# Kernel tuning notes

Measured on AMD Instinct MI355X. Metric: run time of the kernel, lower is better.

## Reference

```python
import jax, jax.numpy as jnp
import numpy as np

N = 50000   # nodes
R = 3       # relations
E = 300000  # edges per relation
H, D = 4, 32  # heads, per-head dim (hidden_feat=128)
IN, HID, OUT = 128, 128, 64
SLOPE = 0.2  # DGL GATConv leaky_relu negative slope


def setup_inputs() -> dict:
    key = jax.random.key(0)
    ks = jax.random.split(key, 12)
    s = 0.05
    return {
        "x": jax.random.normal(ks[0], (N, IN), jnp.float32),
        "edges": jax.random.randint(ks[1], (R, 2, E), 0, N, jnp.int64),
        "W1": jax.random.normal(ks[2], (R, IN, H * D), jnp.float32) * s,
        "al1": jax.random.normal(ks[3], (R, H, D), jnp.float32) * s,
        "ar1": jax.random.normal(ks[4], (R, H, D), jnp.float32) * s,
        "b1": jnp.zeros((R, H, D), jnp.float32),
        "W2": jax.random.normal(ks[5], (R, HID, H * D), jnp.float32) * s,
        "al2": jax.random.normal(ks[6], (R, H, D), jnp.float32) * s,
        "ar2": jax.random.normal(ks[7], (R, H, D), jnp.float32) * s,
        "b2": jnp.zeros((R, H, D), jnp.float32),
        "Wl": jax.random.normal(ks[8], (HID, OUT), jnp.float32) * s,
        "bl": jnp.zeros((OUT,), jnp.float32),
    }


def rgat_layer(h, edges, W, al, ar, b):
    """HeteroGraphConv(sum) of per-relation GATConv. h: [N,F]. Returns [N,H,D]."""
    out = jnp.zeros((N, H, D), h.dtype)
    for r in range(R):  # small fixed relation count
        src, dst = edges[r, 0], edges[r, 1]
        feat = (h @ W[r]).reshape(N, H, D)                  # per-relation projection
        el = jnp.einsum("nhd,hd->nh", feat, al[r])          # [N,H]
        er = jnp.einsum("nhd,hd->nh", feat, ar[r])          # [N,H]
        e = jax.nn.leaky_relu(el[src] + er[dst], SLOPE)      # [E,H]
        # edge softmax over incoming edges per destination node
        emax = jax.ops.segment_max(e, dst, num_segments=N)   # [N,H]
        ex = jnp.exp(e - emax[dst])
        denom = jax.ops.segment_sum(ex, dst, num_segments=N) # [N,H]
        alpha = ex / denom[dst]                               # [E,H]
        msg = feat[src] * alpha[:, :, None]                   # [E,H,D]
        out = out + jax.ops.segment_sum(msg, dst, num_segments=N) + b[r]
    return out


def reference(x, edges, W1, al1, ar1, b1, W2, al2, ar2, b2, Wl, bl):
    h = rgat_layer(x, edges, W1, al1, ar1, b1).reshape(N, H * D)
    h = jax.nn.relu(h)  # dropout is identity in eval mode
    h = rgat_layer(h, edges, W2, al2, ar2, b2).reshape(N, H * D)
    return h @ Wl + bl  # [N, OUT]
```

## Files before the change

### kernel.cpp

```cpp
#include <hip/hip_runtime.h>
#include <hip/hip_bf16.h>
#include <hip/hip_fp16.h>

#define Nn 50000
#define RR 3
#define EE 300000

typedef __attribute__((ext_vector_type(8))) short short8;
typedef __attribute__((ext_vector_type(4))) short short4v;
typedef __attribute__((ext_vector_type(4))) float floatx4;

__device__ __forceinline__ short f2bf(float f) {
    __hip_bfloat16 h = __float2bfloat16(f);
    return *reinterpret_cast<short*>(&h);
}


__global__ void init_kernel(const float* __restrict__ W1, const float* __restrict__ W2,
                            short* __restrict__ Z, int* __restrict__ counts,
                            int* __restrict__ totals) {
    int bx = blockIdx.x;
    if (bx < 586) {
        int i = bx * 256 + threadIdx.x;
        if (i < RR * Nn) counts[i] = 0;
        if (i < 4) totals[i] = 0;
    } else {
        int idx = (bx - 586) * 256 + threadIdx.x;
        if (idx >= 12288) return;
        int lane = idx & 63;
        int nt = (idx >> 6) & 7;
        int kt = (idx >> 9) & 3;
        int rl = idx >> 11;
        int layer = rl / 3, r = rl % 3;
        const float* W = (layer ? W2 : W1) + (size_t)r * 16384;
        int n = nt * 16 + (lane & 15);
        int k0 = kt * 32 + (lane >> 4) * 8;
        short8 v;
        #pragma unroll
        for (int j = 0; j < 8; ++j) v[j] = f2bf(W[(size_t)(k0 + j) * 128 + n]);
        *(short8*)&Z[(size_t)idx * 8] = v;
    }
}


__global__ void count_kernel(const int* __restrict__ edges, int* __restrict__ counts,
                             int* __restrict__ ord) {
    int i = blockIdx.x * blockDim.x + threadIdx.x;
    if (i >= RR * EE / 4) return;
    int g = i * 4;
    int r = g / EE, e0 = g - r * EE;
    int4 d = *(const int4*)&edges[(size_t)r * 2 * EE + EE + e0];
    int* cb = counts + r * Nn;
    int4 o;
    o.x = atomicAdd(&cb[d.x], 1);
    o.y = atomicAdd(&cb[d.y], 1);
    o.z = atomicAdd(&cb[d.z], 1);
    o.w = atomicAdd(&cb[d.w], 1);
    *(int4*)&ord[g] = o;
}

__global__ __launch_bounds__(256) void alloc_kernel(const int* __restrict__ counts,
                                                    int* __restrict__ row_start,
                                                    int* __restrict__ totals) {
    __shared__ int s[256];
    __shared__ int base_s;
    int r = blockIdx.y;
    int tid = threadIdx.x;
    int n = blockIdx.x * 256 + tid;
    int idx = r * Nn + n;
    int c = (n < Nn) ? counts[idx] : 0;
    s[tid] = c;
    __syncthreads();
    #pragma unroll
    for (int off = 1; off < 256; off <<= 1) {
        int v = 0;
        if (tid >= off) v = s[tid - off];
        __syncthreads();
        if (tid >= off) s[tid] += v;
        __syncthreads();
    }
    if (tid == 255) base_s = atomicAdd(&totals[r], s[255]);
    __syncthreads();
    if (n < Nn) row_start[idx] = base_s + s[tid] - c;
}

__global__ void scatter_kernel(const int* __restrict__ edges, const int* __restrict__ ord,
                               const int* __restrict__ row_start,
                               int* __restrict__ csr_s, int* __restrict__ csr_d) {
    int i = blockIdx.x * blockDim.x + threadIdx.x;
    if (i >= RR * EE / 4) return;
    int g = i * 4;
    int r = g / EE, e0 = g - r * EE;
    int4 s4 = *(const int4*)&edges[(size_t)r * 2 * EE + e0];
    int4 d4 = *(const int4*)&edges[(size_t)r * 2 * EE + EE + e0];
    int4 o4 = *(const int4*)&ord[g];
    const int* rs = row_start + r * Nn;
    int* cs = csr_s + (size_t)r * EE;
    int* cd = csr_d + (size_t)r * EE;
    int p0 = rs[d4.x] + o4.x, p1 = rs[d4.y] + o4.y;
    int p2 = rs[d4.z] + o4.z, p3 = rs[d4.w] + o4.w;
    cs[p0] = s4.x; cs[p1] = s4.y; cs[p2] = s4.z; cs[p3] = s4.w;
    cd[p0] = d4.x; cd[p1] = d4.y; cd[p2] = d4.z; cd[p3] = d4.w;
}


template<bool RELU_A>
__global__ __launch_bounds__(256) void gemm_proj_mfma(const float* __restrict__ A,
                                                      const short* __restrict__ Z,
                                                      __half* __restrict__ C) {
    __shared__ short A_lds[64 * 136];
    int tid = threadIdx.x;
    int row0 = blockIdx.x * 64;
    #pragma unroll
    for (int p = 0; p < 8; ++p) {
        int f = p * 256 + tid;
        int row = f >> 5;
        int c4 = (f & 31) * 4;
        float4 v = make_float4(0.f, 0.f, 0.f, 0.f);
        if (row0 + row < Nn) v = *(const float4*)&A[(size_t)(row0 + row) * 128 + c4];
        if (RELU_A) {
            v.x = fmaxf(v.x, 0.f); v.y = fmaxf(v.y, 0.f);
            v.z = fmaxf(v.z, 0.f); v.w = fmaxf(v.w, 0.f);
        }
        short4v sv;
        sv[0] = f2bf(v.x); sv[1] = f2bf(v.y); sv[2] = f2bf(v.z); sv[3] = f2bf(v.w);
        *(short4v*)&A_lds[row * 136 + c4] = sv;
    }
    __syncthreads();
    int wave = tid >> 6, lane = tid & 63;
    int m = lane & 15, q = lane >> 4;
    short8 af[4];
    #pragma unroll
    for (int kt = 0; kt < 4; ++kt)
        af[kt] = *(short8*)&A_lds[(wave * 16 + m) * 136 + kt * 32 + q * 8];
    __syncthreads();
    __half* lds_h = (__half*)A_lds;
    for (int r = 0; r < RR; ++r) {
        floatx4 acc[8];
        #pragma unroll
        for (int nt = 0; nt < 8; ++nt) acc[nt] = (floatx4)(0.f);
        const short* Zr = Z + (size_t)r * 16384;
        #pragma unroll
        for (int kt = 0; kt < 4; ++kt) {
            #pragma unroll
            for (int nt = 0; nt < 8; ++nt) {
                short8 bf = *(const short8*)&Zr[(size_t)(kt * 8 + nt) * 512 + lane * 8];
                acc[nt] = __builtin_amdgcn_mfma_f32_16x16x32_bf16(af[kt], bf, acc[nt], 0, 0, 0);
            }
        }
        #pragma unroll
        for (int nt = 0; nt < 8; ++nt) {
            int col = nt * 16 + m;
            #pragma unroll
            for (int reg = 0; reg < 4; ++reg)
                lds_h[(wave * 16 + q * 4 + reg) * 136 + col] = __float2half(acc[nt][reg]);
        }
        __syncthreads();
        __half* Cr = C + (size_t)r * Nn * 128;
        #pragma unroll
        for (int p = 0; p < 4; ++p) {
            int lin = p * 256 + tid;
            int row = lin >> 4, c8 = (lin & 15) * 8;
            if (row0 + row < Nn)
                *(short8*)&Cr[(size_t)(row0 + row) * 128 + c8] = *(short8*)&lds_h[row * 136 + c8];
        }
        __syncthreads();
    }
}


__global__ __launch_bounds__(256) void gemm_final_kernel(const float* __restrict__ A,
                                                         const float* __restrict__ Wl,
                                                         const float* __restrict__ bl,
                                                         float* __restrict__ out) {
    __shared__ float As[16][65];
    __shared__ float Bs[16][65];
    int tid = threadIdx.x;
    int row0 = blockIdx.x * 64;
    float acc[4][4] = {};
    int tx = tid & 15, ty = tid >> 4;
    for (int k0 = 0; k0 < 128; k0 += 16) {
        {
            int mm = tid >> 2, c = (tid & 3) * 4;
            int row = row0 + mm;
            float4 v = make_float4(0.f, 0.f, 0.f, 0.f);
            if (row < Nn) v = *(const float4*)&A[(size_t)row * 128 + k0 + c];
            As[c + 0][mm] = v.x; As[c + 1][mm] = v.y; As[c + 2][mm] = v.z; As[c + 3][mm] = v.w;
        }
        {
            int kk = tid >> 4, j = (tid & 15) * 4;
            float4 v = *(const float4*)&Wl[(size_t)(k0 + kk) * 64 + j];
            *(float4*)&Bs[kk][j] = v;
        }
        __syncthreads();
        #pragma unroll
        for (int kk = 0; kk < 16; ++kk) {
            float4 a = *(const float4*)&As[kk][ty * 4];
            float4 b = *(const float4*)&Bs[kk][tx * 4];
            float av[4] = {a.x, a.y, a.z, a.w};
            float bv[4] = {b.x, b.y, b.z, b.w};
            #pragma unroll
            for (int i = 0; i < 4; ++i)
                #pragma unroll
                for (int j = 0; j < 4; ++j) acc[i][j] += av[i] * bv[j];
        }
        __syncthreads();
    }
    float4 bias = *(const float4*)&bl[tx * 4];
    #pragma unroll
    for (int i = 0; i < 4; ++i) {
        int row = row0 + ty * 4 + i;
        if (row >= Nn) continue;
        float4 v = make_float4(acc[i][0] + bias.x, acc[i][1] + bias.y,
                               acc[i][2] + bias.z, acc[i][3] + bias.w);
        *(float4*)&out[(size_t)row * 64 + tx * 4] = v;
    }
}


__global__ void elr_kernel(const __half2* __restrict__ feat2, const float* __restrict__ al,
                           const float* __restrict__ ar, float* __restrict__ el,
                           float* __restrict__ er) {
    int i = blockIdx.x * blockDim.x + threadIdx.x;
    if (i >= RR * Nn * 4) return;
    int h = i & 3;
    int nr = i >> 2;
    int n = nr % Nn;
    int r = nr / Nn;
    const __half2* f = feat2 + ((size_t)(r * Nn + n) * 64 + h * 16);
    const float* alp = al + r * 128 + h * 32;
    const float* arp = ar + r * 128 + h * 32;
    float sl = 0.f, sr = 0.f;
    #pragma unroll
    for (int d = 0; d < 16; ++d) {
        float2 v = __half22float2(f[d]);
        sl += v.x * alp[2 * d] + v.y * alp[2 * d + 1];
        sr += v.x * arp[2 * d] + v.y * arp[2 * d + 1];
    }
    el[i] = sl;
    er[i] = sr;
}


__global__ __launch_bounds__(256) void wexp_kernel(const int* __restrict__ csr_s,
                                                   const int* __restrict__ csr_d,
                                                   const float* __restrict__ el,
                                                   const float* __restrict__ er,
                                                   float* __restrict__ wq) {
    int r = blockIdx.y;
    int k = blockIdx.x * 256 + threadIdx.x;
    if (k >= EE) return;
    size_t gk = (size_t)r * EE + k;
    int es = csr_s[gk], ed = csr_d[gk];
    float4 l4 = *(const float4*)&el[(size_t)(r * Nn + es) * 4];
    float4 r4 = *(const float4*)&er[(size_t)(r * Nn + ed) * 4];
    float lv[4] = {l4.x, l4.y, l4.z, l4.w};
    float rv[4] = {r4.x, r4.y, r4.z, r4.w};
    #pragma unroll
    for (int h = 0; h < 4; ++h) {
        float x = lv[h] + rv[h];
        x = (x > 0.f) ? x : 0.2f * x;
        wq[(size_t)h * (RR * EE) + gk] = __expf(x);
    }
}


__global__ __launch_bounds__(256) void agg_kernel(const __half2* __restrict__ feat2,
                                                  const float* __restrict__ wq,
                                                  const int* __restrict__ csr_s,
                                                  const int* __restrict__ row_start,
                                                  const int* __restrict__ counts,
                                                  const float* __restrict__ b,
                                                  float* __restrict__ out) {
    int wave = threadIdx.x >> 6;
    int lane = threadIdx.x & 63;
    int n = blockIdx.x * 4 + wave;
    if (n >= Nn) return;
    int h = lane >> 4;
    int hl = lane & 15;
    int grp = lane & 48;
    int t2 = lane * 2;
    int cntA[RR], stA[RR], sC[RR];
    float wC[RR];
    #pragma unroll
    for (int r = 0; r < RR; ++r) {
        cntA[r] = counts[r * Nn + n];
        stA[r] = row_start[r * Nn + n];
    }
    #pragma unroll
    for (int r = 0; r < RR; ++r) {
        sC[r] = 0; wC[r] = 0.f;
        if (hl < cntA[r]) {
            int idx = stA[r] + hl;
            sC[r] = csr_s[(size_t)r * EE + idx];
            wC[r] = wq[(size_t)h * (RR * EE) + (size_t)r * EE + idx];
        }
    }
    float accx = b[t2] + b[128 + t2] + b[256 + t2];
    float accy = b[t2 + 1] + b[128 + t2 + 1] + b[256 + t2 + 1];
    #pragma unroll
    for (int r = 0; r < RR; ++r) {
        int cnt = cntA[r];
        if (cnt == 0) continue;
        const __half2* fr = feat2 + (size_t)r * Nn * 64;
        float den = 0.f, numx = 0.f, numy = 0.f;
        int s_l = sC[r];
        float w_l = wC[r];
        int i0 = 0;
        while (true) {
            int mm = cnt - i0; if (mm > 16) mm = 16;
            int j = 0;
            for (; j + 3 < mm; j += 4) {
                int s0 = __shfl(s_l, j);
                int s1 = __shfl(s_l, j + 1);
                int s2 = __shfl(s_l, j + 2);
                int s3 = __shfl(s_l, j + 3);
                float w0 = __shfl(w_l, grp | j);
                float w1 = __shfl(w_l, grp | (j + 1));
                float w2 = __shfl(w_l, grp | (j + 2));
                float w3 = __shfl(w_l, grp | (j + 3));
                __half2 f0 = fr[(size_t)s0 * 64 + lane];
                __half2 f1 = fr[(size_t)s1 * 64 + lane];
                __half2 f2 = fr[(size_t)s2 * 64 + lane];
                __half2 f3 = fr[(size_t)s3 * 64 + lane];
                float2 g0 = __half22float2(f0), g1 = __half22float2(f1);
                float2 g2 = __half22float2(f2), g3 = __half22float2(f3);
                den += (w0 + w1) + (w2 + w3);
                numx += w0 * g0.x + w1 * g1.x + w2 * g2.x + w3 * g3.x;
                numy += w0 * g0.y + w1 * g1.y + w2 * g2.y + w3 * g3.y;
            }
            for (; j < mm; ++j) {
                int s0 = __shfl(s_l, j);
                float w0 = __shfl(w_l, grp | j);
                __half2 f0 = fr[(size_t)s0 * 64 + lane];
                float2 g0 = __half22float2(f0);
                den += w0; numx += w0 * g0.x; numy += w0 * g0.y;
            }
            i0 += 16;
            if (i0 >= cnt) break;
            s_l = 0; w_l = 0.f;
            if (i0 + hl < cnt) {
                int idx = stA[r] + i0 + hl;
                s_l = csr_s[(size_t)r * EE + idx];
                w_l = wq[(size_t)h * (RR * EE) + (size_t)r * EE + idx];
            }
        }
        float inv = 1.f / den;
        accx += numx * inv;
        accy += numy * inv;
    }
    *(float2*)&out[(size_t)n * 128 + t2] = make_float2(accx, accy);
}


extern "C" void kernel_launch(void* const* d_in, const int* in_sizes, int n_in,
                              void* d_out, int out_size, void* d_ws, size_t ws_size,
                              hipStream_t stream) {
    const float* x   = (const float*)d_in[0];
    const int*  edges = (const int*)d_in[1];
    const float* W1  = (const float*)d_in[2];
    const float* al1 = (const float*)d_in[3];
    const float* ar1 = (const float*)d_in[4];
    const float* b1  = (const float*)d_in[5];
    const float* W2  = (const float*)d_in[6];
    const float* al2 = (const float*)d_in[7];
    const float* ar2 = (const float*)d_in[8];
    const float* b2  = (const float*)d_in[9];
    const float* Wl  = (const float*)d_in[10];
    const float* bl  = (const float*)d_in[11];
    float* out = (float*)d_out;

    __half* feat  = (__half*)d_ws;
    short* Z      = (short*)(feat + (size_t)RR * Nn * 128);
    float* el     = (float*)(Z + 98304);
    float* er     = el + (size_t)RR * Nn * 4;
    float* outbuf = er + (size_t)RR * Nn * 4;
    float* wq     = outbuf + (size_t)Nn * 128;
    int* counts    = (int*)(wq + (size_t)4 * RR * EE);
    int* row_start = counts + RR * Nn;
    int* totals    = row_start + RR * Nn;
    int* ord       = totals + 4;
    int* csr_s     = ord + RR * EE;
    int* csr_d     = csr_s + RR * EE;

    const int rowBlocks  = (Nn + 63) / 64;
    const int nodeBlocks = (Nn + 255) / 256;
    const int aggBlocks  = (Nn + 3) / 4;
    const int edgeBlocks = (EE + 255) / 256;
    const int edge4Blocks = (RR * EE / 4 + 255) / 256;

    init_kernel<<<634, 256, 0, stream>>>(W1, W2, Z, counts, totals);
    count_kernel<<<edge4Blocks, 256, 0, stream>>>(edges, counts, ord);
    alloc_kernel<<<dim3(nodeBlocks, RR), 256, 0, stream>>>(counts, row_start, totals);
    scatter_kernel<<<edge4Blocks, 256, 0, stream>>>(edges, ord, row_start, csr_s, csr_d);

    gemm_proj_mfma<false><<<rowBlocks, 256, 0, stream>>>(x, Z, feat);
    elr_kernel<<<(RR * Nn * 4 + 255) / 256, 256, 0, stream>>>((const __half2*)feat, al1, ar1, el, er);
    wexp_kernel<<<dim3(edgeBlocks, RR), 256, 0, stream>>>(csr_s, csr_d, el, er, wq);
    agg_kernel<<<aggBlocks, 256, 0, stream>>>((const __half2*)feat, wq, csr_s, row_start, counts, b1, outbuf);

    gemm_proj_mfma<true><<<rowBlocks, 256, 0, stream>>>(outbuf, Z + 49152, feat);
    elr_kernel<<<(RR * Nn * 4 + 255) / 256, 256, 0, stream>>>((const __half2*)feat, al2, ar2, el, er);
    wexp_kernel<<<dim3(edgeBlocks, RR), 256, 0, stream>>>(csr_s, csr_d, el, er, wq);
    agg_kernel<<<aggBlocks, 256, 0, stream>>>((const __half2*)feat, wq, csr_s, row_start, counts, b2, outbuf);

    gemm_final_kernel<<<rowBlocks, 256, 0, stream>>>(outbuf, Wl, bl, out);
}
```

Before: 379.9 us.

## Fuse attention logit computation into projection GEMM and widen edge kernels

Computes el/er dot products inside the MFMA projection kernel from the fp16 tile already staged in LDS, removing the separate elr kernel and its reread of the projected features. Count and scatter kernels now process eight edges per thread. The aggregation inner loop pads chunks to a multiple of four using zero-weight lanes, which removes the scalar tail loop. Costs are extra LDS and per-block work in the GEMM, and redundant loads of node 0 for padded edges.

New measurement: 343.9 us. 1.1x faster.

```diff
diff --git a/kernel.cpp b/kernel.cpp
--- a/kernel.cpp
+++ b/kernel.cpp
@@ -46,17 +46,24 @@
 __global__ void count_kernel(const int* __restrict__ edges, int* __restrict__ counts,
                              int* __restrict__ ord) {
     int i = blockIdx.x * blockDim.x + threadIdx.x;
-    if (i >= RR * EE / 4) return;
-    int g = i * 4;
+    if (i >= RR * EE / 8) return;
+    int g = i * 8;
     int r = g / EE, e0 = g - r * EE;
-    int4 d = *(const int4*)&edges[(size_t)r * 2 * EE + EE + e0];
+    const int* db = &edges[(size_t)r * 2 * EE + EE + e0];
+    int4 d0 = *(const int4*)db;
+    int4 d1 = *(const int4*)(db + 4);
     int* cb = counts + r * Nn;
-    int4 o;
-    o.x = atomicAdd(&cb[d.x], 1);
-    o.y = atomicAdd(&cb[d.y], 1);
-    o.z = atomicAdd(&cb[d.z], 1);
-    o.w = atomicAdd(&cb[d.w], 1);
-    *(int4*)&ord[g] = o;
+    int4 o0, o1;
+    o0.x = atomicAdd(&cb[d0.x], 1);
+    o0.y = atomicAdd(&cb[d0.y], 1);
+    o0.z = atomicAdd(&cb[d0.z], 1);
+    o0.w = atomicAdd(&cb[d0.w], 1);
+    o1.x = atomicAdd(&cb[d1.x], 1);
+    o1.y = atomicAdd(&cb[d1.y], 1);
+    o1.z = atomicAdd(&cb[d1.z], 1);
+    o1.w = atomicAdd(&cb[d1.w], 1);
+    *(int4*)&ord[g] = o0;
+    *(int4*)&ord[g + 4] = o1;
 }
 
 __global__ __launch_bounds__(256) void alloc_kernel(const int* __restrict__ counts,
@@ -88,29 +95,42 @@
                                const int* __restrict__ row_start,
                                int* __restrict__ csr_s, int* __restrict__ csr_d) {
     int i = blockIdx.x * blockDim.x + threadIdx.x;
-    if (i >= RR * EE / 4) return;
-    int g = i * 4;
+    if (i >= RR * EE / 8) return;
+    int g = i * 8;
     int r = g / EE, e0 = g - r * EE;
-    int4 s4 = *(const int4*)&edges[(size_t)r * 2 * EE + e0];
-    int4 d4 = *(const int4*)&edges[(size_t)r * 2 * EE + EE + e0];
-    int4 o4 = *(const int4*)&ord[g];
+    const int* sb = &edges[(size_t)r * 2 * EE + e0];
+    const int* db = sb + EE;
+    int4 s0 = *(const int4*)sb, s1 = *(const int4*)(sb + 4);
+    int4 d0 = *(const int4*)db, d1 = *(const int4*)(db + 4);
+    int4 o0 = *(const int4*)&ord[g], o1 = *(const int4*)&ord[g + 4];
     const int* rs = row_start + r * Nn;
     int* cs = csr_s + (size_t)r * EE;
     int* cd = csr_d + (size_t)r * EE;
-    int p0 = rs[d4.x] + o4.x, p1 = rs[d4.y] + o4.y;
-    int p2 = rs[d4.z] + o4.z, p3 = rs[d4.w] + o4.w;
-    cs[p0] = s4.x; cs[p1] = s4.y; cs[p2] = s4.z; cs[p3] = s4.w;
-    cd[p0] = d4.x; cd[p1] = d4.y; cd[p2] = d4.z; cd[p3] = d4.w;
+    int p0 = rs[d0.x] + o0.x, p1 = rs[d0.y] + o0.y;
+    int p2 = rs[d0.z] + o0.z, p3 = rs[d0.w] + o0.w;
+    int p4 = rs[d1.x] + o1.x, p5 = rs[d1.y] + o1.y;
+    int p6 = rs[d1.z] + o1.z, p7 = rs[d1.w] + o1.w;
+    cs[p0] = s0.x; cs[p1] = s0.y; cs[p2] = s0.z; cs[p3] = s0.w;
+    cs[p4] = s1.x; cs[p5] = s1.y; cs[p6] = s1.z; cs[p7] = s1.w;
+    cd[p0] = d0.x; cd[p1] = d0.y; cd[p2] = d0.z; cd[p3] = d0.w;
+    cd[p4] = d1.x; cd[p5] = d1.y; cd[p6] = d1.z; cd[p7] = d1.w;
 }
 
 
 template<bool RELU_A>
 __global__ __launch_bounds__(256) void gemm_proj_mfma(const float* __restrict__ A,
                                                       const short* __restrict__ Z,
-                                                      __half* __restrict__ C) {
+                                                      const float* __restrict__ al,
+                                                      const float* __restrict__ ar,
+                                                      __half* __restrict__ C,
+                                                      float* __restrict__ el,
+                                                      float* __restrict__ er) {
     __shared__ short A_lds[64 * 136];
+    __shared__ float al_lds[384], ar_lds[384];
     int tid = threadIdx.x;
     int row0 = blockIdx.x * 64;
+    if (tid < 128) { al_lds[256 + tid] = al[256 + tid]; ar_lds[256 + tid] = ar[256 + tid]; }
+    al_lds[tid] = al[tid]; ar_lds[tid] = ar[tid];
     #pragma unroll
     for (int p = 0; p < 8; ++p) {
         int f = p * 256 + tid;
@@ -135,6 +155,8 @@
         af[kt] = *(short8*)&A_lds[(wave * 16 + m) * 136 + kt * 32 + q * 8];
     __syncthreads();
     __half* lds_h = (__half*)A_lds;
+    int row8 = tid >> 2;
+    int hh = tid & 3;
     for (int r = 0; r < RR; ++r) {
         floatx4 acc[8];
         #pragma unroll
@@ -163,6 +185,23 @@
             int row = lin >> 4, c8 = (lin & 15) * 8;
             if (row0 + row < Nn)
                 *(short8*)&Cr[(size_t)(row0 + row) * 128 + c8] = *(short8*)&lds_h[row * 136 + c8];
+        }
+        {
+            const __half2* fp = (const __half2*)&lds_h[row8 * 136 + hh * 32];
+            const float* alp = &al_lds[r * 128 + hh * 32];
+            const float* arp = &ar_lds[r * 128 + hh * 32];
+            float sl = 0.f, sr = 0.f;
+            #pragma unroll
+            for (int d = 0; d < 16; ++d) {
+                float2 v = __half22float2(fp[d]);
+                sl += v.x * alp[2 * d] + v.y * alp[2 * d + 1];
+                sr += v.x * arp[2 * d] + v.y * arp[2 * d + 1];
+            }
+            if (row0 + row8 < Nn) {
+                size_t ei = (size_t)(r * Nn + row0 + row8) * 4 + hh;
+                el[ei] = sl;
+                er[ei] = sr;
+            }
         }
         __syncthreads();
     }
@@ -218,30 +257,6 @@
 }
 
 
-__global__ void elr_kernel(const __half2* __restrict__ feat2, const float* __restrict__ al,
-                           const float* __restrict__ ar, float* __restrict__ el,
-                           float* __restrict__ er) {
-    int i = blockIdx.x * blockDim.x + threadIdx.x;
-    if (i >= RR * Nn * 4) return;
-    int h = i & 3;
-    int nr = i >> 2;
-    int n = nr % Nn;
-    int r = nr / Nn;
-    const __half2* f = feat2 + ((size_t)(r * Nn + n) * 64 + h * 16);
-    const float* alp = al + r * 128 + h * 32;
-    const float* arp = ar + r * 128 + h * 32;
-    float sl = 0.f, sr = 0.f;
-    #pragma unroll
-    for (int d = 0; d < 16; ++d) {
-        float2 v = __half22float2(f[d]);
-        sl += v.x * alp[2 * d] + v.y * alp[2 * d + 1];
-        sr += v.x * arp[2 * d] + v.y * arp[2 * d + 1];
-    }
-    el[i] = sl;
-    er[i] = sr;
-}
-
-
 __global__ __launch_bounds__(256) void wexp_kernel(const int* __restrict__ csr_s,
                                                    const int* __restrict__ csr_d,
                                                    const float* __restrict__ el,
@@ -309,8 +324,8 @@
         int i0 = 0;
         while (true) {
             int mm = cnt - i0; if (mm > 16) mm = 16;
-            int j = 0;
-            for (; j + 3 < mm; j += 4) {
+            int mm4 = (mm + 3) & ~3;
+            for (int j = 0; j < mm4; j += 4) {
                 int s0 = __shfl(s_l, j);
                 int s1 = __shfl(s_l, j + 1);
                 int s2 = __shfl(s_l, j + 2);
@@ -329,13 +344,6 @@
                 numx += w0 * g0.x + w1 * g1.x + w2 * g2.x + w3 * g3.x;
                 numy += w0 * g0.y + w1 * g1.y + w2 * g2.y + w3 * g3.y;
             }
-            for (; j < mm; ++j) {
-                int s0 = __shfl(s_l, j);
-                float w0 = __shfl(w_l, grp | j);
-                __half2 f0 = fr[(size_t)s0 * 64 + lane];
-                float2 g0 = __half22float2(f0);
-                den += w0; numx += w0 * g0.x; numy += w0 * g0.y;
-            }
             i0 += 16;
             if (i0 >= cnt) break;
             s_l = 0; w_l = 0.f;
@@ -387,20 +395,18 @@
     const int nodeBlocks = (Nn + 255) / 256;
     const int aggBlocks  = (Nn + 3) / 4;
     const int edgeBlocks = (EE + 255) / 256;
-    const int edge4Blocks = (RR * EE / 4 + 255) / 256;
+    const int edge8Blocks = (RR * EE / 8 + 255) / 256;
 
     init_kernel<<<634, 256, 0, stream>>>(W1, W2, Z, counts, totals);
-    count_kernel<<<edge4Blocks, 256, 0, stream>>>(edges, counts, ord);
+    count_kernel<<<edge8Blocks, 256, 0, stream>>>(edges, counts, ord);
     alloc_kernel<<<dim3(nodeBlocks, RR), 256, 0, stream>>>(counts, row_start, totals);
-    scatter_kernel<<<edge4Blocks, 256, 0, stream>>>(edges, ord, row_start, csr_s, csr_d);
-
-    gemm_proj_mfma<false><<<rowBlocks, 256, 0, stream>>>(x, Z, feat);
-    elr_kernel<<<(RR * Nn * 4 + 255) / 256, 256, 0, stream>>>((const __half2*)feat, al1, ar1, el, er);
+    scatter_kernel<<<edge8Blocks, 256, 0, stream>>>(edges, ord, row_start, csr_s, csr_d);
+
+    gemm_proj_mfma<false><<<rowBlocks, 256, 0, stream>>>(x, Z, al1, ar1, feat, el, er);
     wexp_kernel<<<dim3(edgeBlocks, RR), 256, 0, stream>>>(csr_s, csr_d, el, er, wq);
     agg_kernel<<<aggBlocks, 256, 0, stream>>>((const __half2*)feat, wq, csr_s, row_start, counts, b1, outbuf);
 
-    gemm_proj_mfma<true><<<rowBlocks, 256, 0, stream>>>(outbuf, Z + 49152, feat);
-    elr_kernel<<<(RR * Nn * 4 + 255) / 256, 256, 0, stream>>>((const __half2*)feat, al2, ar2, el, er);
+    gemm_proj_mfma<true><<<rowBlocks, 256, 0, stream>>>(outbuf, Z + 49152, al2, ar2, feat, el, er);
     wexp_kernel<<<dim3(edgeBlocks, RR), 256, 0, stream>>>(csr_s, csr_d, el, er, wq);
     agg_kernel<<<aggBlocks, 256, 0, stream>>>((const __half2*)feat, wq, csr_s, row_start, counts, b2, outbuf);
 
```
